# Optimization experiments

Measured on AMD Instinct MI355X. Metric: run time of the kernel, lower is better.

The kernel has to match this reference:

```python
import jax, jax.numpy as jnp
import numpy as np

B, T, N, FI, FO = 4, 8, 1024, 64, 64
ALPHA = 0.2          # LeakyReLU negative slope
NEG_INF = -1e12      # matches torch's -1000000000000.0


def setup_inputs() -> dict:
    key = jax.random.key(0)
    k0, k1, k2, k3, k4 = jax.random.split(key, 5)
    inp = jax.random.normal(k0, (B, T, N, FI), dtype=jnp.float32)
    u = jax.random.uniform(k1, (T, N, N), dtype=jnp.float32)
    adj = jnp.where(u > 0.9, u, 0.0)
    # att_mask: [batch, node, seq] in {0,1}
    att_mask = (jax.random.uniform(k2, (B, N, T)) > 0.2).astype(jnp.float32)
    # xavier-ish init (gain 1.414)
    W = jax.random.normal(k3, (FI, FO), dtype=jnp.float32) * (1.414 * np.sqrt(2.0 / (FI + FO)))
    a = jax.random.normal(k4, (2 * FO, 1), dtype=jnp.float32) * (1.414 * np.sqrt(2.0 / (2 * FO + 1)))
    return {"adj": adj, "inp": inp, "att_mask": att_mask, "W": W, "a": a}


def reference(adj, inp, att_mask, W, a):
    Fo = W.shape[1]
    h = jnp.einsum('btnf,fo->btno', inp, W)               # [B,T,N,Fo]
    # additive decomposition of a^T [h_i || h_j] = a1.h_i + a2.h_j
    a1 = a[:Fo, 0]
    a2 = a[Fo:, 0]
    s1 = jnp.einsum('btno,o->btn', h, a1)                 # contributes along rows (i)
    s2 = jnp.einsum('btno,o->btn', h, a2)                 # contributes along cols (j)
    e = s1[..., :, None] + s2[..., None, :]               # [B,T,N,N]
    e = jnp.where(e > 0, e, ALPHA * e)                    # LeakyReLU
    att = jnp.where(adj > 0, e * adj, NEG_INF)            # adj broadcasts over batch
    att = jax.nn.softmax(att, axis=-1)
    m = jnp.transpose(att_mask, (0, 2, 1))                # [B,T,N]
    att = att * (m[..., :, None] * m[..., None, :])       # outer-product mask
    # dropout is identity in eval mode
    h_prime = jnp.einsum('btij,btjo->btio', att, h)       # [B,T,N,Fo]
    return jax.nn.elu(h_prime)                            # concat=True path
```

## Files before the change

kernel.cpp:

```cpp
#include <hip/hip_runtime.h>
#include <hip/hip_bf16.h>
#include <math.h>

#define N_NODES 1024
#define T_DIM 8

typedef __bf16 bf16x8 __attribute__((ext_vector_type(8)));
typedef float  f32x4  __attribute__((ext_vector_type(4)));

__device__ __forceinline__ float readlane_f(float v, int l) {
    return __uint_as_float(__builtin_amdgcn_readlane(__float_as_uint(v), l));
}

__global__ __launch_bounds__(256) void gat_h_kernel(
    const float* __restrict__ inp, const float* __restrict__ W,
    const float* __restrict__ a, const float* __restrict__ att_mask,
    __bf16* __restrict__ hF, float* __restrict__ s1w, float* __restrict__ s2w)
{
    __shared__ float Wl[64 * 64];
    __shared__ float xl[64 * 64];
    __shared__ __bf16 htl[64 * 72];

    const int tid  = threadIdx.x;
    const int blk  = blockIdx.x;
    const int t    = blk & 7;
    const int r_   = blk >> 3;
    const int b    = r_ & 3;
    const int nt   = r_ >> 2;
    const int bt   = b * 8 + t;
    const int n0   = nt * 64;
    const int lane = tid & 63;
    const int wave = tid >> 6;

    const float4* W4  = (const float4*)W;
    float4*       Wl4 = (float4*)Wl;
    const float4* x4  = (const float4*)(inp + (size_t)(bt * N_NODES + n0) * 64);
    float4*       xl4 = (float4*)xl;
#pragma unroll
    for (int k = 0; k < 4; ++k) {
        Wl4[tid + k * 256] = W4[tid + k * 256];
        xl4[tid + k * 256] = x4[tid + k * 256];
    }
    const float a1 = a[lane];
    const float a2 = a[64 + lane];
    __syncthreads();

#pragma unroll 1
    for (int rg = 0; rg < 16; rg += 4) {
        float xr[4], acc[4];
#pragma unroll
        for (int q = 0; q < 4; ++q) {
            xr[q]  = xl[(wave * 16 + rg + q) * 64 + lane];
            acc[q] = 0.f;
        }
#pragma unroll
        for (int f = 0; f < 64; ++f) {
            float w = Wl[f * 64 + lane];
#pragma unroll
            for (int q = 0; q < 4; ++q)
                acc[q] = fmaf(readlane_f(xr[q], f), w, acc[q]);
        }
#pragma unroll
        for (int q = 0; q < 4; ++q) {
            const int r = wave * 16 + rg + q;
            float v1 = acc[q] * a1, v2 = acc[q] * a2;
#pragma unroll
            for (int off = 32; off; off >>= 1) {
                v1 += __shfl_xor(v1, off, 64);
                v2 += __shfl_xor(v2, off, 64);
            }
            if (lane == 0) {
                s1w[bt * N_NODES + n0 + r] = v1;
                s2w[bt * N_NODES + n0 + r] = v2;
            }
            const float mjr = att_mask[((size_t)b * N_NODES + n0 + r) * T_DIM + t];
            htl[lane * 72 + r] = (__bf16)(acc[q] * mjr);
        }
    }
    __syncthreads();

    {
        const int l  = tid & 63;
        const int w  = tid >> 6;
        __bf16* tbase = hF + (size_t)(bt * 16 + nt) * 4096;
#pragma unroll
        for (int cc = 0; cc < 2; ++cc) {
            const int c  = w + cc * 4;
            const int nc = c & 3;
            const int kc = c >> 2;
            bf16x8 v = *(const bf16x8*)&htl[(nc * 16 + (l & 15)) * 72
                                            + (l >> 4) * 8 + kc * 32];
            *(bf16x8*)(tbase + (c * 64 + l) * 8) = v;
        }
    }
}

__global__ __launch_bounds__(512) void gat_attn_kernel(
    const float* __restrict__ adj, const float* __restrict__ att_mask,
    const __bf16* __restrict__ hF, const float* __restrict__ s1w,
    const float* __restrict__ s2w, float* __restrict__ out)
{
    __shared__ __align__(16) __bf16 p_l[8][16 * 72];

    const int blk   = blockIdx.x;
    const int t     = blk & 7;
    const int r_    = blk >> 3;
    const int b     = r_ & 3;
    const int ig    = r_ >> 2;
    const int wave  = threadIdx.x >> 6;
    const int lane  = threadIdx.x & 63;
    const int itile = ig * 8 + wave;
    const int bt    = b * 8 + t;
    const int irow0 = itile * 16;
    const int l15   = lane & 15;
    const int quad  = lane >> 4;

    f32x4 acc[4];
#pragma unroll
    for (int nc = 0; nc < 4; ++nc) acc[nc] = (f32x4){0.f, 0.f, 0.f, 0.f};
    float lsum[16], s1v[16];
#pragma unroll
    for (int r = 0; r < 16; ++r) {
        lsum[r] = 0.f;
        s1v[r]  = s1w[bt * N_NODES + irow0 + r];
    }

    const float*  adjrow = adj + (size_t)t * N_NODES * N_NODES
                               + (size_t)irow0 * N_NODES + lane;
    const __bf16* htb    = hF + (size_t)bt * 16 * 4096 + lane * 8;
    const float*  s2bt   = s2w + bt * N_NODES;
    __bf16* pwr = &p_l[wave][0] + lane;
    const __bf16* prd = &p_l[wave][0] + l15 * 72 + quad * 8;

    float  adj0[16], adj1[16];
    bf16x8 hc[8];
    float  s2c;
    {
#pragma unroll
        for (int r = 0; r < 16; ++r) {
            adj0[r] = adjrow[(size_t)r * N_NODES];
            adj1[r] = adjrow[(size_t)r * N_NODES + 64];
        }
#pragma unroll
        for (int c = 0; c < 8; ++c) hc[c] = *(const bf16x8*)(htb + c * 512);
        s2c = s2bt[lane];
    }

#pragma unroll 2
    for (int it = 0; it < 16; ++it) {
        const int jt1 = (it + 1) & 15;
        const int jt2 = (it + 2) & 15;

        float  adjn[16];
        bf16x8 hn[8];
#pragma unroll
        for (int r = 0; r < 16; ++r)
            adjn[r] = adjrow[(size_t)r * N_NODES + jt2 * 64];
        const __bf16* hp = htb + (size_t)jt1 * 4096;
#pragma unroll
        for (int c = 0; c < 8; ++c) hn[c] = *(const bf16x8*)(hp + c * 512);
        const float s2n = s2bt[jt1 * 64 + lane];

#pragma unroll
        for (int r = 0; r < 16; ++r) {
            float e = s1v[r] + s2c;
            e = fmaxf(e, 0.2f * e);
            float p = (adj0[r] > 0.f) ? __expf(e * adj0[r]) : 0.f;
            lsum[r] += p;
            pwr[r * 72] = (__bf16)p;
        }

        bf16x8 af0 = *(const bf16x8*)(prd);
        bf16x8 af1 = *(const bf16x8*)(prd + 32);
#pragma unroll
        for (int nc = 0; nc < 4; ++nc)
            acc[nc] = __builtin_amdgcn_mfma_f32_16x16x32_bf16(af0, hc[nc], acc[nc], 0, 0, 0);
#pragma unroll
        for (int nc = 0; nc < 4; ++nc)
            acc[nc] = __builtin_amdgcn_mfma_f32_16x16x32_bf16(af1, hc[4 + nc], acc[nc], 0, 0, 0);

#pragma unroll
        for (int r = 0; r < 16; ++r) { adj0[r] = adj1[r]; adj1[r] = adjn[r]; }
#pragma unroll
        for (int c = 0; c < 8; ++c) hc[c] = hn[c];
        s2c = s2n;
    }

#pragma unroll
    for (int r = 0; r < 16; ++r) {
#pragma unroll
        for (int off = 32; off; off >>= 1)
            lsum[r] += __shfl_xor(lsum[r], off, 64);
    }
#pragma unroll
    for (int reg = 0; reg < 4; ++reg) {
        float ls = (quad == 0) ? lsum[reg] : (quad == 1) ? lsum[4 + reg]
                 : (quad == 2) ? lsum[8 + reg] : lsum[12 + reg];
        const int i = irow0 + quad * 4 + reg;
        float mi    = att_mask[((size_t)b * N_NODES + i) * T_DIM + t];
        float scale = mi / ls;
#pragma unroll
        for (int nc = 0; nc < 4; ++nc) {
            float v = acc[nc][reg] * scale;
            v = (v > 0.f) ? v : (__expf(v) - 1.f);
            out[((size_t)bt * N_NODES + i) * 64 + nc * 16 + l15] = v;
        }
    }
}

extern "C" void kernel_launch(void* const* d_in, const int* in_sizes, int n_in,
                              void* d_out, int out_size, void* d_ws, size_t ws_size,
                              hipStream_t stream) {
    (void)in_sizes; (void)n_in; (void)out_size; (void)ws_size;
    const float* adj      = (const float*)d_in[0];
    const float* inp      = (const float*)d_in[1];
    const float* att_mask = (const float*)d_in[2];
    const float* W        = (const float*)d_in[3];
    const float* a        = (const float*)d_in[4];
    float* out = (float*)d_out;

    __bf16* hF  = (__bf16*)d_ws;
    float*  s1w = (float*)((char*)d_ws + (size_t)4 * 1024 * 1024);
    float*  s2w = s1w + 32 * N_NODES;

    gat_h_kernel<<<512, 256, 0, stream>>>(inp, W, a, att_mask, hF, s1w, s2w);
    gat_attn_kernel<<<256, 512, 0, stream>>>(adj, att_mask, hF, s1w, s2w, out);
}
```

Measured before the change: 126.3 us.

## Split attention j-range across two waves per row tile and reduce in LDS

The attention kernel now launches 2048 blocks of 128 threads instead of 256 blocks of 512. Each block handles one 16-row tile, and its two waves each cover half of the column tiles, combining partial accumulators and row sums through shared memory. This is a split-K over j that raises the number of independent blocks and waves to fill the GPU better. The h prefetch depth drops from two tiles to loading the current tile in-loop, and s1 values are made wave-uniform with readfirstlane. The cost is an extra LDS reduction and barrier, plus less latency hiding for the h loads.

```diff
diff --git a/kernel.cpp b/kernel.cpp
--- a/kernel.cpp
+++ b/kernel.cpp
@@ -10,6 +10,9 @@
 
 __device__ __forceinline__ float readlane_f(float v, int l) {
     return __uint_as_float(__builtin_amdgcn_readlane(__float_as_uint(v), l));
+}
+__device__ __forceinline__ float firstlane_f(float v) {
+    return __uint_as_float(__builtin_amdgcn_readfirstlane(__float_as_uint(v)));
 }
 
 __global__ __launch_bounds__(256) void gat_h_kernel(
@@ -95,25 +98,27 @@
     }
 }
 
-__global__ __launch_bounds__(512) void gat_attn_kernel(
+__global__ __launch_bounds__(128, 3) void gat_attn_kernel(
     const float* __restrict__ adj, const float* __restrict__ att_mask,
     const __bf16* __restrict__ hF, const float* __restrict__ s1w,
     const float* __restrict__ s2w, float* __restrict__ out)
 {
-    __shared__ __align__(16) __bf16 p_l[8][16 * 72];
+    __shared__ __align__(16) __bf16 p_l[2][16 * 72];
+    __shared__ __align__(16) float  cacc[64 * 16];
+    __shared__ float clsum[16];
 
     const int blk   = blockIdx.x;
     const int t     = blk & 7;
     const int r_    = blk >> 3;
     const int b     = r_ & 3;
-    const int ig    = r_ >> 2;
+    const int itile = r_ >> 2;
+    const int bt    = b * 8 + t;
+    const int irow0 = itile * 16;
     const int wave  = threadIdx.x >> 6;
     const int lane  = threadIdx.x & 63;
-    const int itile = ig * 8 + wave;
-    const int bt    = b * 8 + t;
-    const int irow0 = itile * 16;
     const int l15   = lane & 15;
     const int quad  = lane >> 4;
+    const int jt0   = wave * 8;
 
     f32x4 acc[4];
 #pragma unroll
@@ -122,7 +127,7 @@
 #pragma unroll
     for (int r = 0; r < 16; ++r) {
         lsum[r] = 0.f;
-        s1v[r]  = s1w[bt * N_NODES + irow0 + r];
+        s1v[r]  = firstlane_f(s1w[bt * N_NODES + irow0 + r]);
     }
 
     const float*  adjrow = adj + (size_t)t * N_NODES * N_NODES
@@ -132,34 +137,30 @@
     __bf16* pwr = &p_l[wave][0] + lane;
     const __bf16* prd = &p_l[wave][0] + l15 * 72 + quad * 8;
 
-    float  adj0[16], adj1[16];
-    bf16x8 hc[8];
-    float  s2c;
+    float adj0[16];
+    float s2c;
     {
 #pragma unroll
-        for (int r = 0; r < 16; ++r) {
-            adj0[r] = adjrow[(size_t)r * N_NODES];
-            adj1[r] = adjrow[(size_t)r * N_NODES + 64];
-        }
-#pragma unroll
-        for (int c = 0; c < 8; ++c) hc[c] = *(const bf16x8*)(htb + c * 512);
-        s2c = s2bt[lane];
+        for (int r = 0; r < 16; ++r)
+            adj0[r] = adjrow[(size_t)r * N_NODES + jt0 * 64];
+        s2c = s2bt[jt0 * 64 + lane];
     }
 
 #pragma unroll 2
-    for (int it = 0; it < 16; ++it) {
-        const int jt1 = (it + 1) & 15;
-        const int jt2 = (it + 2) & 15;
-
-        float  adjn[16];
-        bf16x8 hn[8];
+    for (int it = 0; it < 8; ++it) {
+        const int jc = jt0 + it;
+        const int jn = jt0 + ((it + 1) & 7);
+
+        float adjn[16];
 #pragma unroll
         for (int r = 0; r < 16; ++r)
-            adjn[r] = adjrow[(size_t)r * N_NODES + jt2 * 64];
-        const __bf16* hp = htb + (size_t)jt1 * 4096;
-#pragma unroll
-        for (int c = 0; c < 8; ++c) hn[c] = *(const bf16x8*)(hp + c * 512);
-        const float s2n = s2bt[jt1 * 64 + lane];
+            adjn[r] = adjrow[(size_t)r * N_NODES + jn * 64];
+        const float s2n = s2bt[jn * 64 + lane];
+
+        bf16x8 hc[8];
+        const __bf16* hp = htb + (size_t)jc * 4096;
+#pragma unroll
+        for (int c = 0; c < 8; ++c) hc[c] = *(const bf16x8*)(hp + c * 512);
 
 #pragma unroll
         for (int r = 0; r < 16; ++r) {
@@ -180,9 +181,7 @@
             acc[nc] = __builtin_amdgcn_mfma_f32_16x16x32_bf16(af1, hc[4 + nc], acc[nc], 0, 0, 0);
 
 #pragma unroll
-        for (int r = 0; r < 16; ++r) { adj0[r] = adj1[r]; adj1[r] = adjn[r]; }
-#pragma unroll
-        for (int c = 0; c < 8; ++c) hc[c] = hn[c];
+        for (int r = 0; r < 16; ++r) adj0[r] = adjn[r];
         s2c = s2n;
     }
 
@@ -192,18 +191,43 @@
         for (int off = 32; off; off >>= 1)
             lsum[r] += __shfl_xor(lsum[r], off, 64);
     }
-#pragma unroll
-    for (int reg = 0; reg < 4; ++reg) {
-        float ls = (quad == 0) ? lsum[reg] : (quad == 1) ? lsum[4 + reg]
-                 : (quad == 2) ? lsum[8 + reg] : lsum[12 + reg];
-        const int i = irow0 + quad * 4 + reg;
-        float mi    = att_mask[((size_t)b * N_NODES + i) * T_DIM + t];
-        float scale = mi / ls;
-#pragma unroll
-        for (int nc = 0; nc < 4; ++nc) {
-            float v = acc[nc][reg] * scale;
-            v = (v > 0.f) ? v : (__expf(v) - 1.f);
-            out[((size_t)bt * N_NODES + i) * 64 + nc * 16 + l15] = v;
+
+    if (wave == 1) {
+        float* cb = cacc + lane * 16;
+#pragma unroll
+        for (int nc = 0; nc < 4; ++nc)
+#pragma unroll
+            for (int reg = 0; reg < 4; ++reg)
+                cb[nc * 4 + reg] = acc[nc][reg];
+        if (lane == 0) {
+#pragma unroll
+            for (int r = 0; r < 16; ++r) clsum[r] = lsum[r];
+        }
+    }
+    __syncthreads();
+    if (wave == 0) {
+        const float* cb = cacc + lane * 16;
+#pragma unroll
+        for (int nc = 0; nc < 4; ++nc)
+#pragma unroll
+            for (int reg = 0; reg < 4; ++reg)
+                acc[nc][reg] += cb[nc * 4 + reg];
+#pragma unroll
+        for (int r = 0; r < 16; ++r) lsum[r] += clsum[r];
+
+#pragma unroll
+        for (int reg = 0; reg < 4; ++reg) {
+            float ls = (quad == 0) ? lsum[reg] : (quad == 1) ? lsum[4 + reg]
+                     : (quad == 2) ? lsum[8 + reg] : lsum[12 + reg];
+            const int i = irow0 + quad * 4 + reg;
+            float mi    = att_mask[((size_t)b * N_NODES + i) * T_DIM + t];
+            float scale = mi / ls;
+#pragma unroll
+            for (int nc = 0; nc < 4; ++nc) {
+                float v = acc[nc][reg] * scale;
+                v = (v > 0.f) ? v : (__expf(v) - 1.f);
+                out[((size_t)bt * N_NODES + i) * 64 + nc * 16 + l15] = v;
+            }
         }
     }
 }
@@ -224,5 +248,5 @@
     float*  s2w = s1w + 32 * N_NODES;
 
     gat_h_kernel<<<512, 256, 0, stream>>>(inp, W, a, att_mask, hF, s1w, s2w);
-    gat_attn_kernel<<<256, 512, 0, stream>>>(adj, att_mask, hF, s1w, s2w, out);
-}
+    gat_attn_kernel<<<2048, 128, 0, stream>>>(adj, att_mask, hF, s1w, s2w, out);
+}
```

Result: no change. 127.0 us (+0.5%).
